# Kernel optimization log

Hardware: AMD Instinct MI355X
Metric: run time of the kernel (lower is better)

## Reference

```python
import jax, jax.numpy as jnp
import numpy as np

B, L_PROG = 8, 12
NUM_CLASSES, NUM_ATTRS = 256, 256
MAX_CONCEPTS, MAX_OBJECTS = 4096, 128
N_ATTR_PER_OBJ = 8
E, A, H = 64, 64, 256  # embed_dim, attention_dim, hidden_dim


def setup_inputs() -> dict:
    key = jax.random.key(0)
    ks = jax.random.split(key, 22)
    f = lambda k, shape: jax.random.normal(k, shape, dtype=jnp.float32) * 0.05
    return {
        'class_embIn': f(ks[0], (NUM_CLASSES, E)),
        'class_embOut': f(ks[1], (NUM_CLASSES, E)),
        'attr_embIn': f(ks[2], (NUM_ATTRS, E)),
        'attr_embOut': f(ks[3], (NUM_ATTRS, E)),
        'concept_embIn': f(ks[4], (MAX_CONCEPTS, E)),
        'concept_embOut': f(ks[5], (MAX_CONCEPTS, E)),
        'meta_init': f(ks[6], (A,)),
        'object_init': f(ks[7], (E,)),
        'attention_init': f(ks[8], (A,)),
        'axon_w1': f(ks[9], (A + E, H)), 'axon_b1': f(ks[10], (H,)),
        'axon_w2': f(ks[11], (H, E)), 'axon_b2': f(ks[12], (E,)),
        'meta_w1': f(ks[13], (E + A, H)), 'meta_b1': f(ks[14], (H,)),
        'meta_w2': f(ks[15], (H, A)), 'meta_b2': f(ks[16], (A,)),
        'program_ops': jax.random.randint(ks[17], (B, L_PROG), 0, 3),
        'program_args': jax.random.randint(ks[18], (B, L_PROG), 0, MAX_CONCEPTS),
        'gt_classes': jax.random.randint(ks[19], (B, MAX_OBJECTS), 0, NUM_CLASSES),
        'gt_attributes': jax.random.randint(ks[20], (B, MAX_OBJECTS, N_ATTR_PER_OBJ), 0, NUM_ATTRS),
    }


def _mlp(x, w1, b1, w2, b2):
    return jnp.maximum(x @ w1 + b1, 0.0) @ w2 + b2


def reference(class_embIn, class_embOut, attr_embIn, attr_embOut,
              concept_embIn, concept_embOut, meta_init, object_init,
              attention_init, axon_w1, axon_b1, axon_w2, axon_b2,
              meta_w1, meta_b1, meta_w2, meta_b2,
              program_ops, program_args, gt_classes, gt_attributes):
    Bb, Lp = program_ops.shape
    C = concept_embIn.shape[0]
    N = C + gt_classes.shape[1]  # dim_concept = max_concepts + max_objects

    # object embeddings: class embedding + sum of attribute embeddings  (B, O, E)
    objIn = class_embIn[gt_classes] + attr_embIn[gt_attributes].sum(axis=2)
    objOut = class_embOut[gt_classes] + attr_embOut[gt_attributes].sum(axis=2)

    # thought = [concepts ; objects]  (B, N, E)
    thoughtIn = jnp.concatenate(
        [jnp.broadcast_to(concept_embIn[None], (Bb, C, E)), objIn], axis=1)
    thoughtOut = jnp.concatenate(
        [jnp.broadcast_to(concept_embOut[None], (Bb, C, E)), objOut], axis=1)

    args_emb = concept_embOut[program_args]          # (B, L, E)
    is_mode = (program_ops == 0).astype(jnp.float32)     # (B, L)
    is_insert = (program_ops == 1).astype(jnp.float32)
    is_transfer = (program_ops == 2).astype(jnp.float32)

    meta0 = jnp.broadcast_to(meta_init[None], (Bb, A))
    att0 = jnp.broadcast_to(attention_init[None, None], (Bb, N, A))

    def step(carry, xs):
        meta, attention = carry
        m, ins, tr, arg = xs  # (B,), (B,), (B,), (B,E)
        new_meta = _mlp(jnp.concatenate([meta, arg], axis=-1),
                        meta_w1, meta_b1, meta_w2, meta_b2)
        meta = m[:, None] * new_meta + (1.0 - m[:, None]) * meta
        # insert: meta scaled by mean_e(arg * thoughtOut)
        proj = (arg[:, None, :] * thoughtOut).mean(axis=-1)        # (B, N)
        att_insert = meta[:, None, :] * proj[:, :, None]           # (B, N, A)
        # transfer: bilinear scores thoughtIn . axon, mean-aggregate attention
        mb = jnp.broadcast_to(meta[:, None, :], (Bb, N, A))
        axon = _mlp(jnp.concatenate([thoughtOut, mb], axis=-1),
                    axon_w1, axon_b1, axon_w2, axon_b2)            # (B, N, E)
        scores = jnp.einsum('bje,bke->bjk', thoughtIn, axon)       # (B, N, N)
        att_transfer = jnp.einsum('bjk,bka->bja', scores, attention) / N
        attention = attention + ins[:, None, None] * att_insert \
                              + tr[:, None, None] * att_transfer
        return (meta, attention), None

    xs = (is_mode.T, is_insert.T, is_transfer.T,
          jnp.transpose(args_emb, (1, 0, 2)))
    (meta, attention), _ = jax.lax.scan(step, (meta0, att0), xs)

    output_length = jnp.mean(attention ** 2, axis=-1)              # (B, N)
    return jax.nn.log_softmax(output_length, axis=1)
```

## Files before the change

kernel.cpp:

```cpp
#include <hip/hip_runtime.h>
#include <hip/hip_bf16.h>

typedef __hip_bfloat16 bf16;
typedef float f32x4 __attribute__((ext_vector_type(4)));
typedef short s16x8 __attribute__((ext_vector_type(8)));

#define B_    8
#define LP    12
#define NC    4096
#define NO    128
#define NAPO  8
#define NN    4224
#define E_    64
#define A_    64
#define H_    256
#define QC    80
#define PROJ0 65
#define NCHUNK 17

#define TOT_IN 688896
#define QTF_C  67584
#define QTF_B  337920
#define TB_P   983040

struct Ptr16 { const void* p[16]; };
union U8 { s16x8 v; unsigned u[4]; };

__device__ __forceinline__ float b2f(bf16 x){ return __bfloat162float(x); }
__device__ __forceinline__ float bs2f(unsigned short s){
  union { unsigned u; float f; } x; x.u = ((unsigned)s) << 16; return x.f;
}
__device__ __forceinline__ unsigned short f2bs(float f){
  bf16 h = __float2bfloat16(f);
  union { bf16 h; unsigned short s; } x; x.h = h; return x.s;
}
__device__ __forceinline__ unsigned pack2(float a, float b){
  return (unsigned)f2bs(a) | ((unsigned)f2bs(b) << 16);
}
__device__ __forceinline__ float lo16f(unsigned w){
  union { unsigned u; float f; } x; x.u = w << 16; return x.f;
}
__device__ __forceinline__ float hi16f(unsigned w){
  union { unsigned u; float f; } x; x.u = w & 0xffff0000u; return x.f;
}
__device__ __forceinline__ float rdval(const void* p, int i, int fl){
  return fl ? ((const float*)p)[i] : bs2f(((const unsigned short*)p)[i]);
}

__global__ void k_prep(Ptr16 ps, int* flag, float* dst,
                       unsigned short* awFrag,
                       const int* gtc, const int* gta,
                       float* objIn, float* objOut, float* qsum_esum){
  int tid = threadIdx.x;
  const unsigned short* u = (const unsigned short*)ps.p[4];
  int hit = (((u[tid*16] >> 7) & 0xFF) >= 137) ? 1 : 0;
  unsigned long long m = __ballot(hit);
  int fl = (m != 0ULL) ? 1 : 0;
  int mb = blockIdx.x;
  if (mb < 2691){
    int idx = mb*256 + tid;
    if (idx >= TOT_IN) return;
    constexpr int cum[17] = {0,16384,32768,49152,65536,327680,589824,589888,589952,
                             622720,622976,639360,639424,672192,672448,688832,688896};
    int t = 0;
    #pragma unroll
    for (int i=1;i<16;i++) if (idx >= cum[i]) t = i;
    dst[idx] = rdval(ps.p[t], idx - cum[t], fl);
  } else if (mb < 2755){
    int idx = (mb-2691)*256 + tid;
    int j = idx & 7;
    int lane = (idx >> 3) & 63;
    int mm = (idx >> 9) & 15;
    int kc = idx >> 13;
    int e = kc*32 + (lane>>4)*8 + j;
    int h = mm*16 + (lane&15);
    awFrag[idx] = f2bs(rdval(ps.p[8], e*H_ + h, fl));
  } else if (mb < 3011){
    int idx = (mb-2755)*256 + tid;
    int e = idx & 63; int bo = idx >> 6;
    int cls = gtc[bo];
    float vi = rdval(ps.p[0], cls*E_ + e, fl);
    float vo = rdval(ps.p[1], cls*E_ + e, fl);
    const int* ga = gta + bo*NAPO;
    #pragma unroll
    for (int j=0;j<NAPO;j++){
      int at = ga[j];
      vi += rdval(ps.p[2], at*E_ + e, fl);
      vo += rdval(ps.p[3], at*E_ + e, fl);
    }
    objIn[idx] = vi; objOut[idx] = vo;
  } else {
    if (tid < 656) qsum_esum[tid] = 0.f;
    if (tid == 0) *flag = fl;
  }
}

__device__ __forceinline__ void mid_meta(char* smem, int b,
                       const float* conceptOut, const float* meta_init,
                       const float* mw1, const float* mb1, const float* mw2, const float* mb2,
                       const float* aw1, const float* ab1,
                       const int* ops, const int* args,
                       float* metaAll, float* metaH){
  unsigned* mw1p = (unsigned*)smem;
  unsigned* mw2p = (unsigned*)(smem + 65536);
  unsigned* aw1p = (unsigned*)(smem + 98304);
  float* meta_s  = (float*)(smem + 131072);
  float* argx    = (float*)(smem + 131328);
  float* hid     = (float*)(smem + 131584);
  float* part    = (float*)(smem + 132608);
  int tid = threadIdx.x;

  for (int i=tid; i<64*256; i+=256){
    int j2 = i >> 8, t = i & 255;
    mw1p[i] = pack2(mw1[(2*j2)*H_ + t], mw1[(2*j2+1)*H_ + t]);
  }
  for (int i=tid; i<128*64; i+=256){
    int h2 = i >> 6, a = i & 63;
    mw2p[i] = pack2(mw2[(2*h2)*A_ + a], mw2[(2*h2+1)*A_ + a]);
  }
  for (int i=tid; i<32*256; i+=256){
    int a2 = i >> 8, t = i & 255;
    aw1p[i] = pack2(aw1[(E_+2*a2)*H_ + t], aw1[(E_+2*a2+1)*H_ + t]);
  }
  float r_mb1 = mb1[tid];
  float r_ab1 = ab1[tid];
  float r_mb2 = (tid < A_) ? mb2[tid] : 0.f;
  if (tid < A_) meta_s[tid] = meta_init[tid];
  __syncthreads();

  for (int t=0;t<LP;t++){
    int op  = ops[b*LP + t];
    int arg = args[b*LP + t];
    if (tid >= 64 && tid < 128) argx[tid-64] = conceptOut[arg*E_ + (tid-64)];
    __syncthreads();
    float acc = r_mb1;
    for (int j2=0;j2<32;j2++){
      unsigned w = mw1p[j2*256 + tid];
      float2 xp = *(const float2*)&meta_s[2*j2];
      acc = fmaf(xp.x, lo16f(w), acc);
      acc = fmaf(xp.y, hi16f(w), acc);
    }
    for (int j2=0;j2<32;j2++){
      unsigned w = mw1p[(32+j2)*256 + tid];
      float2 xp = *(const float2*)&argx[2*j2];
      acc = fmaf(xp.x, lo16f(w), acc);
      acc = fmaf(xp.y, hi16f(w), acc);
    }
    hid[tid] = fmaxf(acc, 0.f);
    __syncthreads();
    int wv_ = tid >> 6, l = tid & 63;
    float acc2 = 0.f;
    for (int h2 = wv_*32; h2 < wv_*32+32; h2++){
      unsigned w = mw2p[h2*64 + l];
      float2 hp = *(const float2*)&hid[2*h2];
      acc2 = fmaf(hp.x, lo16f(w), acc2);
      acc2 = fmaf(hp.y, hi16f(w), acc2);
    }
    part[wv_*64 + l] = acc2;
    __syncthreads();
    if (tid < A_){
      float s = part[tid] + part[64+tid] + part[128+tid] + part[192+tid] + r_mb2;
      float nm = (op==0) ? s : meta_s[tid];
      meta_s[tid] = nm;
      metaAll[(b*LP+t)*A_ + tid] = nm;
    }
    __syncthreads();
    float mh = r_ab1;
    for (int a2=0;a2<32;a2++){
      unsigned w = aw1p[a2*256 + tid];
      float2 mp = *(const float2*)&meta_s[2*a2];
      mh = fmaf(mp.x, lo16f(w), mh);
      mh = fmaf(mp.y, hi16f(w), mh);
    }
    metaH[(b*LP+t)*H_ + tid] = mh;
  }
}

__device__ __forceinline__ void mid_qt(char* smem, int idx,
                       const float* conceptIn, const float* conceptOut, const int* args,
                       const float* objIn, const float* objOut,
                       unsigned short* QTf, float* qsum){
  float* tile = (float*)smem;
  float* argv = (float*)(smem + 66560);
  float* qs   = (float*)(smem + 69632);
  int b = idx / NCHUNK, chunk = idx % NCHUNK;
  int tid = threadIdx.x;
  int rows = (chunk < 16) ? 256 : 128;
  int n0 = chunk*256;
  int n = n0 + tid;
  bool valid = (tid < rows);
  if (tid < 80) qs[tid] = 0.f;
  unsigned short* Qb = QTf + (size_t)b*QTF_B + ((n>>5)*512 + (n&31));
  {
    const float* src = (chunk < 16) ? (conceptIn + (size_t)n0*E_) : (objIn + (size_t)b*NO*E_);
    int tot = rows*64;
    for (int i=tid; i<tot; i+=256) tile[(i>>6)*65 + (i&63)] = src[i];
  }
  __syncthreads();
  if (valid){
    Qb[0] = 0x3F80;
    Qb[4*QTF_C + 13*32] = 0;
    Qb[4*QTF_C + 14*32] = 0;
    Qb[4*QTF_C + 15*32] = 0;
    for (int e=0;e<64;e++){
      int qc = 1+e;
      Qb[(qc>>4)*QTF_C + (qc&15)*32] = f2bs(tile[tid*65 + e]);
    }
    for (int i=0;i<64;i++){
      int e = (i + tid) & 63;
      atomicAdd(&qs[1+e], tile[tid*65+e]);
    }
  }
  __syncthreads();
  for (int i=tid;i<LP*E_;i+=256) argv[i] = conceptOut[args[b*LP + (i>>6)]*E_ + (i&63)];
  {
    const float* src = (chunk < 16) ? (conceptOut + (size_t)n0*E_) : (objOut + (size_t)b*NO*E_);
    int tot = rows*64;
    for (int i=tid; i<tot; i+=256) tile[(i>>6)*65 + (i&63)] = src[i];
  }
  __syncthreads();
  float dots[LP];
  #pragma unroll
  for (int t=0;t<LP;t++) dots[t] = 0.f;
  for (int e=0;e<64;e++){
    float o = tile[tid*65 + e];
    #pragma unroll
    for (int t=0;t<LP;t++) dots[t] += o*argv[t*64+e];
  }
  #pragma unroll
  for (int t=0;t<LP;t++){
    float v = valid ? dots[t]*(1.f/E_) : 0.f;
    if (valid){
      int qc = PROJ0+t;
      Qb[(qc>>4)*QTF_C + (qc&15)*32] = f2bs(v);
    }
    float r = v;
    #pragma unroll
    for (int off=32; off>0; off>>=1) r += __shfl_down(r, off, 64);
    if ((tid & 63) == 0) atomicAdd(&qs[PROJ0+t], r);
  }
  __syncthreads();
  if (tid < 80) atomicAdd(&qsum[b*QC + tid], qs[tid]);
  if (chunk == 0 && tid == 0) atomicAdd(&qsum[b*QC], (float)NN);
}

__device__ __forceinline__ void mid_base(int blk,
                       const float* conceptOut, const float* objOut,
                       const unsigned short* awFrag,
                       unsigned short* AoptC, unsigned short* AoptO){
  int n0 = blk * 64;
  int tid = threadIdx.x;
  int w = tid >> 6, l = tid & 63, quad = l >> 4, lq = l & 15;
  int n = n0 + w*16 + lq;
  const float* src = (n < NC) ? (conceptOut + (size_t)n*E_) : (objOut + (size_t)(n-NC)*E_);
  f32x4 acc[16];
  #pragma unroll
  for (int m=0;m<16;m++) acc[m] = (f32x4){0.f,0.f,0.f,0.f};
  #pragma unroll
  for (int kc=0;kc<2;kc++){
    s16x8 bfr;
    #pragma unroll
    for (int j=0;j<8;j++) bfr[j] = (short)f2bs(src[kc*32 + quad*8 + j]);
    const unsigned short* ap = awFrag + ((size_t)(kc*16)*64 + l)*8;
    #pragma unroll
    for (int m=0;m<16;m++){
      s16x8 af = *(const s16x8*)(ap + (size_t)m*64*8);
      acc[m] = __builtin_amdgcn_mfma_f32_16x16x32_bf16(af, bfr, acc[m], 0, 0, 0);
    }
  }
  int nl = n & 31;
  if (n < NC){
    int nch = n >> 5;
    #pragma unroll
    for (int m=0;m<16;m++){
      #pragma unroll
      for (int r=0;r<4;r++)
        AoptC[(size_t)(m*128 + nch)*512 + (quad*4+r)*32 + nl] = f2bs(acc[m][r]);
    }
  } else {
    int no = n - NC; int bb = no >> 7; int oc = (no & 127) >> 5;
    #pragma unroll
    for (int m=0;m<16;m++){
      #pragma unroll
      for (int r=0;r<4;r++)
        AoptO[(size_t)((bb*16 + m)*4 + oc)*512 + (quad*4+r)*32 + nl] = f2bs(acc[m][r]);
    }
  }
}

__global__ __launch_bounds__(256) void k_mid(
    const float* conceptIn, const float* conceptOut,
    const float* meta_init, const float* mw1, const float* mb1, const float* mw2, const float* mb2,
    const float* aw1, const float* ab1, const int* ops, const int* args,
    const float* objIn, const float* objOut, const unsigned short* awFrag,
    float* metaAll, float* metaH, unsigned short* QTf, float* qsum,
    unsigned short* AoptC, unsigned short* AoptO){
  __shared__ __align__(16) char smem[133888];
  int mb = blockIdx.x;
  if (mb < 8)
    mid_meta(smem, mb, conceptOut, meta_init, mw1, mb1, mw2, mb2, aw1, ab1, ops, args, metaAll, metaH);
  else if (mb < 144)
    mid_qt(smem, mb-8, conceptIn, conceptOut, args, objIn, objOut, QTf, qsum);
  else
    mid_base(mb-144, conceptOut, objOut, awFrag, AoptC, AoptO);
}

__global__ __launch_bounds__(64) void k_T(const unsigned short* AoptC, const unsigned short* AoptO,
                                          const unsigned short* QTf, const float* metaH,
                                          unsigned* TB){
  int bid = blockIdx.x;
  int kh = bid & 7; int ht = (bid >> 3) & 3; int bt = bid >> 5; int b = bt / LP;
  int l = threadIdx.x, quad = l >> 4, lq = l & 15;
  int off = lq*32 + quad*8;
  int start = (kh < 4) ? (kh*17) : (68 + (kh-4)*16);
  int count = (kh < 4) ? 17 : 16;
  float mh[4];
  #pragma unroll
  for (int s=0;s<4;s++) mh[s] = metaH[(size_t)bt*H_ + ht*64 + s*16 + lq];
  f32x4 acc[4][5];
  #pragma unroll
  for (int s=0;s<4;s++){
    #pragma unroll
    for (int c=0;c<5;c++) acc[s][c] = (f32x4){0.f,0.f,0.f,0.f};
  }
  const unsigned short* QTb = QTf + (size_t)b*QTF_B + off;
  const unsigned short* AC  = AoptC + (size_t)(ht*4)*65536 + off;
  const unsigned short* AO  = AoptO + (size_t)(b*16 + ht*4)*2048 + off;
  for (int it=0; it<count; it++){
    int nchunk = start + it;
    U8 bfr[5];
    #pragma unroll
    for (int c=0;c<5;c++)
      bfr[c].v = *(const s16x8*)(QTb + (size_t)c*QTF_C + (size_t)nchunk*512);
    bool isC = (nchunk < 128);
    #pragma unroll
    for (int s=0;s<4;s++){
      U8 a;
      a.v = isC ? *(const s16x8*)(AC + (size_t)s*65536 + (size_t)nchunk*512)
                : *(const s16x8*)(AO + (size_t)s*2048 + (size_t)(nchunk-128)*512);
      float mhs = mh[s];
      U8 af;
      #pragma unroll
      for (int d=0;d<4;d++){
        unsigned wv = a.u[d];
        float lo = fmaxf(__uint_as_float(wv << 16) + mhs, 0.f);
        float hi = fmaxf(__uint_as_float(wv & 0xffff0000u) + mhs, 0.f);
        af.u[d] = __builtin_amdgcn_perm(__float_as_uint(hi), __float_as_uint(lo), 0x07060302u);
      }
      #pragma unroll
      for (int c=0;c<5;c++)
        acc[s][c] = __builtin_amdgcn_mfma_f32_16x16x32_bf16(af.v, bfr[c].v, acc[s][c], 0, 0, 0);
    }
  }
  unsigned* Tp = TB + (size_t)kh*TB_P + ((size_t)bt*4 + ht)*2560;
  #pragma unroll
  for (int s=0;s<4;s++){
    #pragma unroll
    for (int c=0;c<5;c++){
      uint2 v;
      v.x = pack2(acc[s][c][0], acc[s][c][1]);
      v.y = pack2(acc[s][c][2], acc[s][c][3]);
      *(uint2*)(Tp + (s*5+c)*128 + l*2) = v;
    }
  }
}

__global__ __launch_bounds__(256) void k_U(const unsigned* TB,
                                           const float* w2, const float* b2v,
                                           const float* qsum, float* Ut0, float* Ut1){
  __shared__ float Wt[128*64];
  __shared__ float Tt[128*81];
  int bid = blockIdx.x;
  int kq = bid & 1; int bt = bid >> 1; int b = bt / LP;
  int tid = threadIdx.x;
  for (int i=tid; i<8192; i+=256){
    int hl = i >> 6, e = i & 63;
    Wt[i] = w2[(kq*128 + hl)*E_ + e];
  }
  #pragma unroll
  for (int half=0; half<2; half++){
    const unsigned* base = TB + ((size_t)bt*4 + kq*2 + half)*2560;
    for (int i2=tid; i2<2560; i2+=256){
      float lo = 0.f, hi = 0.f;
      #pragma unroll
      for (int p=0;p<8;p++){
        unsigned w = base[(size_t)p*TB_P + i2];
        lo += lo16f(w); hi += hi16f(w);
      }
      int idx = 2*i2;
      int sc = idx >> 8; int ll = (idx >> 2) & 63; int r = idx & 3;
      int s = sc/5, c = sc - s*5;
      int hl = half*64 + s*16 + ((ll>>4)<<2) + r;
      int qc = c*16 + (ll&15);
      Tt[hl*81 + qc]     = lo;
      Tt[(hl+1)*81 + qc] = hi;
    }
  }
  __syncthreads();
  int el = tid & 15, ql = tid >> 4;
  float acc[4][5];
  #pragma unroll
  for (int i=0;i<4;i++){
    #pragma unroll
    for (int j=0;j<5;j++) acc[i][j]=0.f;
  }
  #pragma unroll 4
  for (int kk=0; kk<128; kk++){
    float4 wv = *(const float4*)&Wt[kk*64 + el*4];
    float ww[4] = {wv.x, wv.y, wv.z, wv.w};
    const float* tp = &Tt[kk*81 + ql*5];
    #pragma unroll
    for (int j=0;j<5;j++){
      float tv = tp[j];
      #pragma unroll
      for (int i=0;i<4;i++) acc[i][j] = fmaf(ww[i], tv, acc[i][j]);
    }
  }
  const float invN = 1.f/NN;
  float* Up = (kq ? Ut1 : Ut0) + (size_t)bt*5120;
  if (kq == 0){
    float be[4], qv[5];
    #pragma unroll
    for (int i=0;i<4;i++) be[i] = b2v[el*4+i];
    #pragma unroll
    for (int j=0;j<5;j++) qv[j] = qsum[b*QC + ql*5+j];
    #pragma unroll
    for (int i=0;i<4;i++){
      #pragma unroll
      for (int j=0;j<5;j++)
        Up[(el*4+i)*QC + ql*5+j] = (acc[i][j] + be[i]*qv[j]) * invN;
    }
  } else {
    #pragma unroll
    for (int i=0;i<4;i++){
      #pragma unroll
      for (int j=0;j<5;j++)
        Up[(el*4+i)*QC + ql*5+j] = acc[i][j] * invN;
    }
  }
}

__global__ __launch_bounds__(256) void k_rec(const float* Ut0, const float* Ut1, const float* metaAll,
                                             const int* ops, const float* att_init, float* Cm){
  __shared__ float C[QC*65];
  __shared__ float Ul[2][64*81];
  int b = blockIdx.x, tid = threadIdx.x;
  int w = tid >> 6, l = tid & 63, quad = l >> 4, lq = l & 15;
  for (int i=tid;i<QC*65;i+=256) C[i] = 0.f;
  if (tid < A_) C[tid] = att_init[tid];
  {
    const float* U0 = Ut0 + (size_t)(b*LP)*5120;
    const float* U1 = Ut1 + (size_t)(b*LP)*5120;
    #pragma unroll
    for (int k=0;k<5;k++){
      int i = tid*4 + k*1024;
      float4 v0 = *(const float4*)&U0[i];
      float4 v1 = *(const float4*)&U1[i];
      int r = i/80, c = i%80;
      Ul[0][r*81+c]   = v0.x+v1.x; Ul[0][r*81+c+1] = v0.y+v1.y;
      Ul[0][r*81+c+2] = v0.z+v1.z; Ul[0][r*81+c+3] = v0.w+v1.w;
    }
  }
  __syncthreads();
  for (int t=0;t<LP;t++){
    float4 rv0[5], rv1[5];
    if (t < LP-1){
      const float* U0 = Ut0 + (size_t)(b*LP+t+1)*5120;
      const float* U1 = Ut1 + (size_t)(b*LP+t+1)*5120;
      #pragma unroll
      for (int k=0;k<5;k++){
        rv0[k] = *(const float4*)&U0[tid*4 + k*1024];
        rv1[k] = *(const float4*)&U1[tid*4 + k*1024];
      }
    }
    const float* Uc = Ul[t&1];
    U8 af[3][4];
    #pragma unroll
    for (int k0t=0;k0t<3;k0t++){
      #pragma unroll
      for (int s=0;s<4;s++){
        int e = s*16 + lq;
        int qb = k0t*32 + quad*8;
        float v[8];
        #pragma unroll
        for (int j=0;j<8;j++){
          int qc = qb + j;
          v[j] = (qc < QC) ? Uc[e*81 + qc] : 0.f;
        }
        #pragma unroll
        for (int d=0;d<4;d++) af[k0t][s].u[d] = pack2(v[2*d], v[2*d+1]);
      }
    }
    U8 bf[3];
    #pragma unroll
    for (int k0t=0;k0t<3;k0t++){
      int kb = k0t*32 + quad*8;
      float v[8];
      #pragma unroll
      for (int j=0;j<8;j++){
        int k = kb + j;
        v[j] = (k < QC) ? C[k*65 + w*16 + lq] : 0.f;
      }
      #pragma unroll
      for (int d=0;d<4;d++) bf[k0t].u[d] = pack2(v[2*d], v[2*d+1]);
    }
    f32x4 acc[4];
    #pragma unroll
    for (int s=0;s<4;s++){
      acc[s] = (f32x4){0.f,0.f,0.f,0.f};
      #pragma unroll
      for (int k0t=0;k0t<3;k0t++)
        acc[s] = __builtin_amdgcn_mfma_f32_16x16x32_bf16(af[k0t][s].v, bf[k0t].v, acc[s], 0, 0, 0);
    }
    int op = ops[b*LP + t];
    float tr  = (op==2) ? 1.f : 0.f;
    float ins = (op==1) ? 1.f : 0.f;
    __syncthreads();
    #pragma unroll
    for (int s=0;s<4;s++){
      #pragma unroll
      for (int r=0;r<4;r++){
        int e = s*16 + quad*4 + r;
        C[(1+e)*65 + w*16 + lq] += tr*acc[s][r];
      }
    }
    if (tid < A_) C[(PROJ0+t)*65 + tid] += ins*metaAll[(b*LP+t)*A_ + tid];
    if (t < LP-1){
      float* Un = Ul[(t+1)&1];
      #pragma unroll
      for (int k=0;k<5;k++){
        int i = tid*4 + k*1024;
        int r = i/80, c = i%80;
        Un[r*81+c]   = rv0[k].x+rv1[k].x; Un[r*81+c+1] = rv0[k].y+rv1[k].y;
        Un[r*81+c+2] = rv0[k].z+rv1[k].z; Un[r*81+c+3] = rv0[k].w+rv1[k].w;
      }
    }
    __syncthreads();
  }
  for (int i=tid;i<QC*A_;i+=256) Cm[b*QC*A_ + i] = C[(i>>6)*65 + (i&63)];
}

__global__ __launch_bounds__(128) void k_out(const unsigned short* QTf, const float* Cm,
                                             float* ol, float* esum){
  __shared__ float C[QC*A_];
  __shared__ float wsum[2];
  int b = blockIdx.x / 33, rem = blockIdx.x % 33;
  int tid = threadIdx.x;
  for (int i=tid;i<QC*A_;i+=128) C[i] = Cm[b*QC*A_ + i];
  __syncthreads();
  int n = rem*128 + tid;
  float y[A_];
  #pragma unroll
  for (int a=0;a<A_;a++) y[a]=0.f;
  const unsigned short* Qb = QTf + (size_t)b*QTF_B + ((n>>5)*512 + (n&31));
  for (int j=0;j<QC;j++){
    float qvv = bs2f(Qb[(j>>4)*QTF_C + (j&15)*32]);
    const float* Cj = &C[j*A_];
    #pragma unroll
    for (int a=0;a<A_;a++) y[a] = fmaf(qvv, Cj[a], y[a]);
  }
  float s = 0.f;
  #pragma unroll
  for (int a=0;a<A_;a++) s = fmaf(y[a], y[a], s);
  float o = s * (1.f/A_);
  ol[(size_t)b*NN + n] = o;
  float contrib = expf(o);
  #pragma unroll
  for (int off=32; off>0; off>>=1) contrib += __shfl_down(contrib, off, 64);
  if ((tid & 63) == 0) wsum[tid>>6] = contrib;
  __syncthreads();
  if (tid == 0) atomicAdd(&esum[b], wsum[0]+wsum[1]);
}

__global__ void k_fin(const float* ol, const float* esum, const int* flag, void* out){
  int idx = blockIdx.x*256 + threadIdx.x;
  if (idx < B_*NN){
    int b = idx / NN;
    float v = ol[idx] - logf(esum[b]);
    if (*flag) ((float*)out)[idx] = v;
    else       ((bf16*)out)[idx]  = __float2bfloat16(v);
  }
}

extern "C" void kernel_launch(void* const* d_in, const int* in_sizes, int n_in,
                              void* d_out, int out_size, void* d_ws, size_t ws_size,
                              hipStream_t stream) {
  (void)in_sizes; (void)n_in; (void)out_size; (void)ws_size;
  const int* ops  = (const int*)d_in[17];
  const int* args = (const int*)d_in[18];
  const int* gtc  = (const int*)d_in[19];
  const int* gta  = (const int*)d_in[20];

  float* ws = (float*)d_ws;
  int* flag = (int*)ws;
  float* W  = ws + 16;

  const float* conceptIn  = W + 65536;
  const float* conceptOut = W + 327680;
  const float* meta_init  = W + 589824;
  const float* att_init   = W + 589888;
  const float* aw1        = W + 589952;
  const float* ab1        = W + 622720;
  const float* aw2        = W + 622976;
  const float* ab2        = W + 639360;
  const float* mw1        = W + 639424;
  const float* mb1        = W + 672192;
  const float* mw2        = W + 672448;
  const float* mb2        = W + 688832;

  constexpr size_t OFF_OBJIN   = 16 + TOT_IN;
  constexpr size_t OFF_OBJOUT  = OFF_OBJIN  + 65536;
  constexpr size_t OFF_METAALL = OFF_OBJOUT + 65536;
  constexpr size_t OFF_METAH   = OFF_METAALL + 6144;
  constexpr size_t OFF_QSUM    = OFF_METAH  + 24576;
  constexpr size_t OFF_ESUM    = OFF_QSUM   + 640;
  constexpr size_t OFF_UT0     = OFF_ESUM   + 16;
  constexpr size_t OFF_UT1     = OFF_UT0    + 491520;
  constexpr size_t OFF_CM      = OFF_UT1    + 491520;
  constexpr size_t OFF_OL      = OFF_CM     + 40960;
  constexpr size_t OFF_QTF     = OFF_OL     + 33792;
  constexpr size_t OFF_AOPTC   = OFF_QTF    + 1351680;
  constexpr size_t OFF_AOPTO   = OFF_AOPTC  + 524288;
  constexpr size_t OFF_AWF     = OFF_AOPTO  + 131072;
  constexpr size_t OFF_TB      = OFF_AWF    + 8192;

  float* objIn   = ws + OFF_OBJIN;
  float* objOut  = ws + OFF_OBJOUT;
  float* metaAll = ws + OFF_METAALL;
  float* metaH   = ws + OFF_METAH;
  float* qsum    = ws + OFF_QSUM;
  float* esum    = ws + OFF_ESUM;
  float* Ut0     = ws + OFF_UT0;
  float* Ut1     = ws + OFF_UT1;
  float* Cm      = ws + OFF_CM;
  float* ol      = ws + OFF_OL;
  unsigned short* QTf    = (unsigned short*)(ws + OFF_QTF);
  unsigned short* AoptC  = (unsigned short*)(ws + OFF_AOPTC);
  unsigned short* AoptO  = (unsigned short*)(ws + OFF_AOPTO);
  unsigned short* awFrag = (unsigned short*)(ws + OFF_AWF);
  unsigned* TB           = (unsigned*)(ws + OFF_TB);

  Ptr16 ps;
  const int src_idx[16] = {0,1,2,3,4,5,6,8,9,10,11,12,13,14,15,16};
  for (int i=0;i<16;i++) ps.p[i] = d_in[src_idx[i]];

  k_prep<<<3012, 256, 0, stream>>>(ps, flag, W, awFrag, gtc, gta, objIn, objOut, qsum);
  k_mid <<<224, 256, 0, stream>>>(conceptIn, conceptOut, meta_init, mw1, mb1, mw2, mb2,
                                  aw1, ab1, ops, args, objIn, objOut, awFrag,
                                  metaAll, metaH, QTf, qsum, AoptC, AoptO);
  k_T   <<<B_*LP*4*8, 64, 0, stream>>>(AoptC, AoptO, QTf, metaH, TB);
  k_U   <<<B_*LP*2, 256, 0, stream>>>(TB, aw2, ab2, qsum, Ut0, Ut1);
  k_rec <<<B_, 256, 0, stream>>>(Ut0, Ut1, metaAll, ops, att_init, Cm);
  k_out <<<B_*33, 128, 0, stream>>>(QTf, Cm, ol, esum);
  k_fin <<<(B_*NN + 255)/256, 256, 0, stream>>>(ol, esum, flag, d_out);
}
```

Before: 263.5 us.

## Fuse k_T and k_U into one block-level kernel with LDS split-K reduction

The k_T and k_U kernels become one k_TU kernel. Each 512-thread block runs the eight split-K waves for one (bt, ht) tile and reduces their bf16 partials through shared memory instead of a global TB buffer. The block then applies its 64-row slice of w2 and writes four per-ht partial U tiles. Bias and qsum scaling move into k_rec, which now sums four partials. This removes a kernel launch and the global round trip of TB, at the cost of larger blocks (about 100KB of LDS, so lower occupancy), fewer blocks (384), and w2 read from global memory without LDS staging.

```diff
diff --git a/kernel.cpp b/kernel.cpp
--- a/kernel.cpp
+++ b/kernel.cpp
@@ -21,7 +21,6 @@
 #define TOT_IN 688896
 #define QTF_C  67584
 #define QTF_B  337920
-#define TB_P   983040
 
 struct Ptr16 { const void* p[16]; };
 union U8 { s16x8 v; unsigned u[4]; };
@@ -305,12 +304,17 @@
     mid_base(mb-144, conceptOut, objOut, awFrag, AoptC, AoptO);
 }
 
-__global__ __launch_bounds__(64) void k_T(const unsigned short* AoptC, const unsigned short* AoptO,
-                                          const unsigned short* QTf, const float* metaH,
-                                          unsigned* TB){
+__global__ __launch_bounds__(512) void k_TU(const unsigned short* AoptC, const unsigned short* AoptO,
+                                            const unsigned short* QTf, const float* metaH,
+                                            const float* w2, float* Upart){
+  __shared__ __align__(16) char sm[102912];
+  unsigned* slice = (unsigned*)sm;
+  float* Tsum = (float*)(sm + 81920);
   int bid = blockIdx.x;
-  int kh = bid & 7; int ht = (bid >> 3) & 3; int bt = bid >> 5; int b = bt / LP;
-  int l = threadIdx.x, quad = l >> 4, lq = l & 15;
+  int ht = bid & 3; int bt = bid >> 2; int b = bt / LP;
+  int tid = threadIdx.x;
+  int kh = tid >> 6;
+  int l = tid & 63, quad = l >> 4, lq = l & 15;
   int off = lq*32 + quad*8;
   int start = (kh < 4) ? (kh*17) : (68 + (kh-4)*16);
   int count = (kh < 4) ? 17 : 16;
@@ -352,7 +356,7 @@
         acc[s][c] = __builtin_amdgcn_mfma_f32_16x16x32_bf16(af.v, bfr[c].v, acc[s][c], 0, 0, 0);
     }
   }
-  unsigned* Tp = TB + (size_t)kh*TB_P + ((size_t)bt*4 + ht)*2560;
+  unsigned* Sp = slice + kh*2560;
   #pragma unroll
   for (int s=0;s<4;s++){
     #pragma unroll
@@ -360,117 +364,97 @@
       uint2 v;
       v.x = pack2(acc[s][c][0], acc[s][c][1]);
       v.y = pack2(acc[s][c][2], acc[s][c][3]);
-      *(uint2*)(Tp + (s*5+c)*128 + l*2) = v;
-    }
-  }
-}
-
-__global__ __launch_bounds__(256) void k_U(const unsigned* TB,
-                                           const float* w2, const float* b2v,
-                                           const float* qsum, float* Ut0, float* Ut1){
-  __shared__ float Wt[128*64];
-  __shared__ float Tt[128*81];
-  int bid = blockIdx.x;
-  int kq = bid & 1; int bt = bid >> 1; int b = bt / LP;
-  int tid = threadIdx.x;
-  for (int i=tid; i<8192; i+=256){
-    int hl = i >> 6, e = i & 63;
-    Wt[i] = w2[(kq*128 + hl)*E_ + e];
-  }
-  #pragma unroll
-  for (int half=0; half<2; half++){
-    const unsigned* base = TB + ((size_t)bt*4 + kq*2 + half)*2560;
-    for (int i2=tid; i2<2560; i2+=256){
-      float lo = 0.f, hi = 0.f;
-      #pragma unroll
-      for (int p=0;p<8;p++){
-        unsigned w = base[(size_t)p*TB_P + i2];
-        lo += lo16f(w); hi += hi16f(w);
-      }
-      int idx = 2*i2;
-      int sc = idx >> 8; int ll = (idx >> 2) & 63; int r = idx & 3;
-      int s = sc/5, c = sc - s*5;
-      int hl = half*64 + s*16 + ((ll>>4)<<2) + r;
-      int qc = c*16 + (ll&15);
-      Tt[hl*81 + qc]     = lo;
-      Tt[(hl+1)*81 + qc] = hi;
-    }
-  }
-  __syncthreads();
-  int el = tid & 15, ql = tid >> 4;
-  float acc[4][5];
-  #pragma unroll
-  for (int i=0;i<4;i++){
-    #pragma unroll
-    for (int j=0;j<5;j++) acc[i][j]=0.f;
-  }
-  #pragma unroll 4
-  for (int kk=0; kk<128; kk++){
-    float4 wv = *(const float4*)&Wt[kk*64 + el*4];
-    float ww[4] = {wv.x, wv.y, wv.z, wv.w};
-    const float* tp = &Tt[kk*81 + ql*5];
-    #pragma unroll
-    for (int j=0;j<5;j++){
-      float tv = tp[j];
-      #pragma unroll
-      for (int i=0;i<4;i++) acc[i][j] = fmaf(ww[i], tv, acc[i][j]);
-    }
-  }
-  const float invN = 1.f/NN;
-  float* Up = (kq ? Ut1 : Ut0) + (size_t)bt*5120;
-  if (kq == 0){
-    float be[4], qv[5];
-    #pragma unroll
-    for (int i=0;i<4;i++) be[i] = b2v[el*4+i];
-    #pragma unroll
-    for (int j=0;j<5;j++) qv[j] = qsum[b*QC + ql*5+j];
-    #pragma unroll
-    for (int i=0;i<4;i++){
-      #pragma unroll
-      for (int j=0;j<5;j++)
-        Up[(el*4+i)*QC + ql*5+j] = (acc[i][j] + be[i]*qv[j]) * invN;
-    }
-  } else {
-    #pragma unroll
-    for (int i=0;i<4;i++){
-      #pragma unroll
-      for (int j=0;j<5;j++)
-        Up[(el*4+i)*QC + ql*5+j] = acc[i][j] * invN;
-    }
-  }
-}
-
-__global__ __launch_bounds__(256) void k_rec(const float* Ut0, const float* Ut1, const float* metaAll,
-                                             const int* ops, const float* att_init, float* Cm){
+      *(uint2*)(Sp + (s*5+c)*128 + l*2) = v;
+    }
+  }
+  __syncthreads();
+  #pragma unroll
+  for (int d5=0; d5<5; d5++){
+    int i2 = d5*512 + tid;
+    float lo = 0.f, hi = 0.f;
+    #pragma unroll
+    for (int p=0;p<8;p++){
+      unsigned w = slice[p*2560 + i2];
+      lo += lo16f(w); hi += hi16f(w);
+    }
+    int idx = 2*i2;
+    int sc = idx >> 8; int ll = (idx >> 2) & 63; int r = idx & 3;
+    int s = sc/5, c = sc - s*5;
+    int h = s*16 + ((ll>>4)<<2) + r;
+    int qc = c*16 + (ll&15);
+    Tsum[h*82 + qc]     = lo;
+    Tsum[(h+1)*82 + qc] = hi;
+  }
+  __syncthreads();
+  int e = tid >> 3, qc0 = (tid & 7)*10;
+  float u[10];
+  #pragma unroll
+  for (int j=0;j<10;j++) u[j] = 0.f;
+  const float* wp = w2 + (size_t)(ht*64)*E_ + e;
+  for (int h=0; h<64; h++){
+    float wv = wp[(size_t)h*E_];
+    const float* tp = &Tsum[h*82 + qc0];
+    #pragma unroll
+    for (int j2=0;j2<5;j2++){
+      float2 tv = *(const float2*)&tp[2*j2];
+      u[2*j2]   = fmaf(wv, tv.x, u[2*j2]);
+      u[2*j2+1] = fmaf(wv, tv.y, u[2*j2+1]);
+    }
+  }
+  float* Up = Upart + ((size_t)bt*4 + ht)*5120 + tid*10;
+  #pragma unroll
+  for (int j=0;j<10;j++) Up[j] = u[j];
+}
+
+__global__ __launch_bounds__(256) void k_rec(const float* Upart, const float* metaAll,
+                                             const int* ops, const float* att_init,
+                                             const float* ab2, const float* qsum, float* Cm){
   __shared__ float C[QC*65];
   __shared__ float Ul[2][64*81];
   int b = blockIdx.x, tid = threadIdx.x;
   int w = tid >> 6, l = tid & 63, quad = l >> 4, lq = l & 15;
   for (int i=tid;i<QC*65;i+=256) C[i] = 0.f;
   if (tid < A_) C[tid] = att_init[tid];
+  const float invN = 1.f/NN;
+  float4 bq[5];
+  int roff[5];
+  #pragma unroll
+  for (int k=0;k<5;k++){
+    int i = tid*4 + k*1024;
+    int r = i/80, c = i%80;
+    roff[k] = r*81 + c;
+    float be = ab2[r];
+    float4 qv = *(const float4*)&qsum[b*QC + c];
+    bq[k] = (float4){be*qv.x*invN, be*qv.y*invN, be*qv.z*invN, be*qv.w*invN};
+  }
   {
-    const float* U0 = Ut0 + (size_t)(b*LP)*5120;
-    const float* U1 = Ut1 + (size_t)(b*LP)*5120;
+    const float* U0 = Upart + (size_t)(b*LP)*20480;
     #pragma unroll
     for (int k=0;k<5;k++){
       int i = tid*4 + k*1024;
       float4 v0 = *(const float4*)&U0[i];
-      float4 v1 = *(const float4*)&U1[i];
-      int r = i/80, c = i%80;
-      Ul[0][r*81+c]   = v0.x+v1.x; Ul[0][r*81+c+1] = v0.y+v1.y;
-      Ul[0][r*81+c+2] = v0.z+v1.z; Ul[0][r*81+c+3] = v0.w+v1.w;
+      float4 v1 = *(const float4*)&U0[5120+i];
+      float4 v2 = *(const float4*)&U0[10240+i];
+      float4 v3 = *(const float4*)&U0[15360+i];
+      float* d = &Ul[0][roff[k]];
+      d[0] = (v0.x+v1.x+v2.x+v3.x)*invN + bq[k].x;
+      d[1] = (v0.y+v1.y+v2.y+v3.y)*invN + bq[k].y;
+      d[2] = (v0.z+v1.z+v2.z+v3.z)*invN + bq[k].z;
+      d[3] = (v0.w+v1.w+v2.w+v3.w)*invN + bq[k].w;
     }
   }
   __syncthreads();
   for (int t=0;t<LP;t++){
-    float4 rv0[5], rv1[5];
+    float4 rv0[5], rv1[5], rv2[5], rv3[5];
     if (t < LP-1){
-      const float* U0 = Ut0 + (size_t)(b*LP+t+1)*5120;
-      const float* U1 = Ut1 + (size_t)(b*LP+t+1)*5120;
+      const float* U = Upart + (size_t)(b*LP+t+1)*20480;
       #pragma unroll
       for (int k=0;k<5;k++){
-        rv0[k] = *(const float4*)&U0[tid*4 + k*1024];
-        rv1[k] = *(const float4*)&U1[tid*4 + k*1024];
+        int i = tid*4 + k*1024;
+        rv0[k] = *(const float4*)&U[i];
+        rv1[k] = *(const float4*)&U[5120+i];
+        rv2[k] = *(const float4*)&U[10240+i];
+        rv3[k] = *(const float4*)&U[15360+i];
       }
     }
     const float* Uc = Ul[t&1];
@@ -529,10 +513,11 @@
       float* Un = Ul[(t+1)&1];
       #pragma unroll
       for (int k=0;k<5;k++){
-        int i = tid*4 + k*1024;
-        int r = i/80, c = i%80;
-        Un[r*81+c]   = rv0[k].x+rv1[k].x; Un[r*81+c+1] = rv0[k].y+rv1[k].y;
-        Un[r*81+c+2] = rv0[k].z+rv1[k].z; Un[r*81+c+3] = rv0[k].w+rv1[k].w;
+        float* d = &Un[roff[k]];
+        d[0] = (rv0[k].x+rv1[k].x+rv2[k].x+rv3[k].x)*invN + bq[k].x;
+        d[1] = (rv0[k].y+rv1[k].y+rv2[k].y+rv3[k].y)*invN + bq[k].y;
+        d[2] = (rv0[k].z+rv1[k].z+rv2[k].z+rv3[k].z)*invN + bq[k].z;
+        d[3] = (rv0[k].w+rv1[k].w+rv2[k].w+rv3[k].w)*invN + bq[k].w;
       }
     }
     __syncthreads();
@@ -614,15 +599,13 @@
   constexpr size_t OFF_METAH   = OFF_METAALL + 6144;
   constexpr size_t OFF_QSUM    = OFF_METAH  + 24576;
   constexpr size_t OFF_ESUM    = OFF_QSUM   + 640;
-  constexpr size_t OFF_UT0     = OFF_ESUM   + 16;
-  constexpr size_t OFF_UT1     = OFF_UT0    + 491520;
-  constexpr size_t OFF_CM      = OFF_UT1    + 491520;
+  constexpr size_t OFF_UP     = OFF_ESUM   + 16;
+  constexpr size_t OFF_CM      = OFF_UP     + 1966080;
   constexpr size_t OFF_OL      = OFF_CM     + 40960;
   constexpr size_t OFF_QTF     = OFF_OL     + 33792;
   constexpr size_t OFF_AOPTC   = OFF_QTF    + 1351680;
   constexpr size_t OFF_AOPTO   = OFF_AOPTC  + 524288;
   constexpr size_t OFF_AWF     = OFF_AOPTO  + 131072;
-  constexpr size_t OFF_TB      = OFF_AWF    + 8192;
 
   float* objIn   = ws + OFF_OBJIN;
   float* objOut  = ws + OFF_OBJOUT;
@@ -630,15 +613,13 @@
   float* metaH   = ws + OFF_METAH;
   float* qsum    = ws + OFF_QSUM;
   float* esum    = ws + OFF_ESUM;
-  float* Ut0     = ws + OFF_UT0;
-  float* Ut1     = ws + OFF_UT1;
+  float* Upart   = ws + OFF_UP;
   float* Cm      = ws + OFF_CM;
   float* ol      = ws + OFF_OL;
   unsigned short* QTf    = (unsigned short*)(ws + OFF_QTF);
   unsigned short* AoptC  = (unsigned short*)(ws + OFF_AOPTC);
   unsigned short* AoptO  = (unsigned short*)(ws + OFF_AOPTO);
   unsigned short* awFrag = (unsigned short*)(ws + OFF_AWF);
-  unsigned* TB           = (unsigned*)(ws + OFF_TB);
 
   Ptr16 ps;
   const int src_idx[16] = {0,1,2,3,4,5,6,8,9,10,11,12,13,14,15,16};
@@ -648,9 +629,8 @@
   k_mid <<<224, 256, 0, stream>>>(conceptIn, conceptOut, meta_init, mw1, mb1, mw2, mb2,
                                   aw1, ab1, ops, args, objIn, objOut, awFrag,
                                   metaAll, metaH, QTf, qsum, AoptC, AoptO);
-  k_T   <<<B_*LP*4*8, 64, 0, stream>>>(AoptC, AoptO, QTf, metaH, TB);
-  k_U   <<<B_*LP*2, 256, 0, stream>>>(TB, aw2, ab2, qsum, Ut0, Ut1);
-  k_rec <<<B_, 256, 0, stream>>>(Ut0, Ut1, metaAll, ops, att_init, Cm);
+  k_TU  <<<B_*LP*4, 512, 0, stream>>>(AoptC, AoptO, QTf, metaH, aw2, Upart);
+  k_rec <<<B_, 256, 0, stream>>>(Upart, metaAll, ops, att_init, ab2, qsum, Cm);
   k_out <<<B_*33, 128, 0, stream>>>(QTf, Cm, ol, esum);
   k_fin <<<(B_*NN + 255)/256, 256, 0, stream>>>(ol, esum, flag, d_out);
 }
```

Measured after the change: 282.8 us. +7.3%, slower.

## Fuse recurrence, output projection and log-softmax into one kernel using MFMA

Applied to the files above, without the earlier changes.

Merges k_rec, k_out and k_fin into a single per-batch kernel. The final coefficient matrix C stays in shared memory and is multiplied against QTf with bf16 MFMA instructions instead of scalar fp32 FMAs. The log-softmax normalisation is done in-block, which removes the esum atomics, the Cm/ol global round-trips and two kernel launches. In exchange the output projection now runs on only 8 blocks instead of 264, and C is rounded to bf16, which costs some accuracy.

```diff
diff --git a/kernel.cpp b/kernel.cpp
--- a/kernel.cpp
+++ b/kernel.cpp
@@ -440,10 +440,12 @@
   }
 }
 
-__global__ __launch_bounds__(256) void k_rec(const float* Ut0, const float* Ut1, const float* metaAll,
-                                             const int* ops, const float* att_init, float* Cm){
+__global__ __launch_bounds__(256) void k_rof(const float* Ut0, const float* Ut1, const float* metaAll,
+                                             const int* ops, const float* att_init,
+                                             const unsigned short* QTf, const int* flag, void* out){
   __shared__ float C[QC*65];
   __shared__ float Ul[2][64*81];
+  __shared__ float red[8];
   int b = blockIdx.x, tid = threadIdx.x;
   int w = tid >> 6, l = tid & 63, quad = l >> 4, lq = l & 15;
   for (int i=tid;i<QC*65;i+=256) C[i] = 0.f;
@@ -537,48 +539,70 @@
     }
     __syncthreads();
   }
-  for (int i=tid;i<QC*A_;i+=256) Cm[b*QC*A_ + i] = C[(i>>6)*65 + (i&63)];
-}
-
-__global__ __launch_bounds__(128) void k_out(const unsigned short* QTf, const float* Cm,
-                                             float* ol, float* esum){
-  __shared__ float C[QC*A_];
-  __shared__ float wsum[2];
-  int b = blockIdx.x / 33, rem = blockIdx.x % 33;
-  int tid = threadIdx.x;
-  for (int i=tid;i<QC*A_;i+=128) C[i] = Cm[b*QC*A_ + i];
-  __syncthreads();
-  int n = rem*128 + tid;
-  float y[A_];
-  #pragma unroll
-  for (int a=0;a<A_;a++) y[a]=0.f;
-  const unsigned short* Qb = QTf + (size_t)b*QTF_B + ((n>>5)*512 + (n&31));
-  for (int j=0;j<QC;j++){
-    float qvv = bs2f(Qb[(j>>4)*QTF_C + (j&15)*32]);
-    const float* Cj = &C[j*A_];
-    #pragma unroll
-    for (int a=0;a<A_;a++) y[a] = fmaf(qvv, Cj[a], y[a]);
-  }
-  float s = 0.f;
-  #pragma unroll
-  for (int a=0;a<A_;a++) s = fmaf(y[a], y[a], s);
-  float o = s * (1.f/A_);
-  ol[(size_t)b*NN + n] = o;
-  float contrib = expf(o);
-  #pragma unroll
-  for (int off=32; off>0; off>>=1) contrib += __shfl_down(contrib, off, 64);
-  if ((tid & 63) == 0) wsum[tid>>6] = contrib;
-  __syncthreads();
-  if (tid == 0) atomicAdd(&esum[b], wsum[0]+wsum[1]);
-}
-
-__global__ void k_fin(const float* ol, const float* esum, const int* flag, void* out){
-  int idx = blockIdx.x*256 + threadIdx.x;
-  if (idx < B_*NN){
-    int b = idx / NN;
-    float v = ol[idx] - logf(esum[b]);
-    if (*flag) ((float*)out)[idx] = v;
-    else       ((bf16*)out)[idx]  = __float2bfloat16(v);
+  U8 bfr[3][4];
+  #pragma unroll
+  for (int kk=0;kk<3;kk++){
+    #pragma unroll
+    for (int at=0;at<4;at++){
+      float v[8];
+      #pragma unroll
+      for (int jj=0;jj<8;jj++){
+        int j = kk*32 + quad*8 + jj;
+        v[jj] = (j < QC) ? C[j*65 + at*16 + lq] : 0.f;
+      }
+      #pragma unroll
+      for (int d=0;d<4;d++) bfr[kk][at].u[d] = pack2(v[2*d], v[2*d+1]);
+    }
+  }
+  float* ols = &Ul[0][0];
+  const unsigned short* Qb = QTf + (size_t)b*QTF_B;
+  for (int mt = w; mt < NN/16; mt += 4){
+    int nb = (mt>>1)*512 + (mt&1)*16 + lq;
+    f32x4 acc[4];
+    #pragma unroll
+    for (int at=0;at<4;at++) acc[at] = (f32x4){0.f,0.f,0.f,0.f};
+    #pragma unroll
+    for (int kk=0;kk<3;kk++){
+      U8 af;
+      #pragma unroll
+      for (int d=0;d<4;d++){
+        int j0 = kk*32 + quad*8 + 2*d;
+        int j1 = j0 + 1;
+        unsigned u0 = (j0 < QC) ? (unsigned)Qb[(j0>>4)*QTF_C + (j0&15)*32 + nb] : 0u;
+        unsigned u1 = (j1 < QC) ? (unsigned)Qb[(j1>>4)*QTF_C + (j1&15)*32 + nb] : 0u;
+        af.u[d] = u0 | (u1 << 16);
+      }
+      #pragma unroll
+      for (int at=0;at<4;at++)
+        acc[at] = __builtin_amdgcn_mfma_f32_16x16x32_bf16(af.v, bfr[kk][at].v, acc[at], 0, 0, 0);
+    }
+    #pragma unroll
+    for (int r=0;r<4;r++){
+      float s = 0.f;
+      #pragma unroll
+      for (int at=0;at<4;at++) s = fmaf(acc[at][r], acc[at][r], s);
+      s += __shfl_xor(s, 1, 64);
+      s += __shfl_xor(s, 2, 64);
+      s += __shfl_xor(s, 4, 64);
+      s += __shfl_xor(s, 8, 64);
+      if (lq == 0) ols[mt*16 + quad*4 + r] = s * (1.f/A_);
+    }
+  }
+  __syncthreads();
+  float le = 0.f;
+  for (int n = tid; n < NN; n += 256) le += expf(ols[n]);
+  #pragma unroll
+  for (int off=32; off>0; off>>=1) le += __shfl_down(le, off, 64);
+  if (l == 0) red[w] = le;
+  __syncthreads();
+  if (tid == 0) red[4] = logf(red[0]+red[1]+red[2]+red[3]);
+  __syncthreads();
+  float lg = red[4];
+  int fl = *flag;
+  for (int n = tid; n < NN; n += 256){
+    float v = ols[n] - lg;
+    if (fl) ((float*)out)[(size_t)b*NN + n] = v;
+    else    ((bf16*)out)[(size_t)b*NN + n] = __float2bfloat16(v);
   }
 }
 
@@ -616,9 +640,7 @@
   constexpr size_t OFF_ESUM    = OFF_QSUM   + 640;
   constexpr size_t OFF_UT0     = OFF_ESUM   + 16;
   constexpr size_t OFF_UT1     = OFF_UT0    + 491520;
-  constexpr size_t OFF_CM      = OFF_UT1    + 491520;
-  constexpr size_t OFF_OL      = OFF_CM     + 40960;
-  constexpr size_t OFF_QTF     = OFF_OL     + 33792;
+  constexpr size_t OFF_QTF     = OFF_UT1    + 491520;
   constexpr size_t OFF_AOPTC   = OFF_QTF    + 1351680;
   constexpr size_t OFF_AOPTO   = OFF_AOPTC  + 524288;
   constexpr size_t OFF_AWF     = OFF_AOPTO  + 131072;
@@ -629,11 +651,8 @@
   float* metaAll = ws + OFF_METAALL;
   float* metaH   = ws + OFF_METAH;
   float* qsum    = ws + OFF_QSUM;
-  float* esum    = ws + OFF_ESUM;
   float* Ut0     = ws + OFF_UT0;
   float* Ut1     = ws + OFF_UT1;
-  float* Cm      = ws + OFF_CM;
-  float* ol      = ws + OFF_OL;
   unsigned short* QTf    = (unsigned short*)(ws + OFF_QTF);
   unsigned short* AoptC  = (unsigned short*)(ws + OFF_AOPTC);
   unsigned short* AoptO  = (unsigned short*)(ws + OFF_AOPTO);
@@ -650,7 +669,5 @@
                                   metaAll, metaH, QTf, qsum, AoptC, AoptO);
   k_T   <<<B_*LP*4*8, 64, 0, stream>>>(AoptC, AoptO, QTf, metaH, TB);
   k_U   <<<B_*LP*2, 256, 0, stream>>>(TB, aw2, ab2, qsum, Ut0, Ut1);
-  k_rec <<<B_, 256, 0, stream>>>(Ut0, Ut1, metaAll, ops, att_init, Cm);
-  k_out <<<B_*33, 128, 0, stream>>>(QTf, Cm, ol, esum);
-  k_fin <<<(B_*NN + 255)/256, 256, 0, stream>>>(ol, esum, flag, d_out);
-}
+  k_rof <<<B_, 256, 0, stream>>>(Ut0, Ut1, metaAll, ops, att_init, QTf, flag, d_out);
+}
```

After: 397.4 us. 50.8% more time.
